# Optimization experiments

Hardware: AMD Instinct MI355X
Metric: run time of the kernel (lower is better)

The kernel has to match this reference:

```python
import jax, jax.numpy as jnp
import numpy as np

B, K, V, NB = 256, 62, 14522, 28

def setup_inputs() -> dict:
    key = jax.random.key(0)
    ks = jax.random.split(key, 10)
    thetas = jax.random.normal(ks[0], (B, K * 3), dtype=jnp.float32) * 0.2
    bone_lengths_core = jax.random.normal(ks[1], (B, NB), dtype=jnp.float32)
    center_bone_length = jax.random.uniform(ks[2], (B, 1), dtype=jnp.float32) + 0.5
    trans = jax.random.normal(ks[3], (B, 3), dtype=jnp.float32)
    scale = jax.random.uniform(ks[4], (B,), dtype=jnp.float32) + 0.5
    v_template = jax.random.normal(ks[5], (V, 3), dtype=jnp.float32) * 0.05
    t_pose_joints = jax.random.normal(ks[6], (K, 3), dtype=jnp.float32) * 0.1
    weights = jax.nn.softmax(jax.random.normal(ks[7], (V, K), dtype=jnp.float32) * 2.0, axis=1)
    # kinematic tree: parent[i] < i (binary-ish tree), parent[0] unused
    parents = jnp.maximum((jnp.arange(K) - 1) // 2, 0).astype(jnp.int64)
    bone_length_mapper = jax.random.randint(ks[8], (K,), -1, NB).astype(jnp.int64)
    return {"thetas": thetas, "bone_lengths_core": bone_lengths_core,
            "center_bone_length": center_bone_length, "trans": trans, "scale": scale,
            "v_template": v_template, "t_pose_joints": t_pose_joints, "weights": weights,
            "parents": parents, "bone_length_mapper": bone_length_mapper}

def euler2mat(r):
    # r: [N,3] ZYX euler angles -> [N,3,3]
    z, y, x = r[:, 0], r[:, 1], r[:, 2]
    cx, sx = jnp.cos(x), jnp.sin(x)
    cy, sy = jnp.cos(y), jnp.sin(y)
    cz, sz = jnp.cos(z), jnp.sin(z)
    one = jnp.ones_like(x)
    zero = jnp.zeros_like(x)
    Rx = jnp.stack([one, zero, zero, zero, cx, -sx, zero, sx, cx], -1).reshape(-1, 3, 3)
    Ry = jnp.stack([cy, zero, sy, zero, one, zero, -sy, zero, cy], -1).reshape(-1, 3, 3)
    Rz = jnp.stack([cz, -sz, zero, sz, cz, zero, zero, zero, one], -1).reshape(-1, 3, 3)
    return jnp.einsum('nij,njk,nkl->nil', Rz, Ry, Rx)

def _forward(thetas, bone_lengths_core, center_bone_length, trans, scale,
             v_template, t_pose_joints, weights, parents, bone_length_mapper):
    b = thetas.shape[0]
    k = t_pose_joints.shape[0]
    blc = jax.nn.sigmoid(bone_lengths_core / 5.0) * 2.0          # [B,28]
    R = euler2mat(thetas.reshape(-1, 3)).reshape(b, k, 3, 3)      # [B,K,3,3]
    Jt = t_pose_joints                                            # [K,3]
    # per-joint bone-length scale factor [B,K]
    gathered = blc[:, jnp.clip(bone_length_mapper, 0)]            # [B,K]
    factor = jnp.where(bone_length_mapper[None, :] < 0, 1.0, gathered)
    factor = factor.at[:, 1].set(center_bone_length[:, 0])
    factor = factor.at[:, 0].set(1.0)
    # local translations: root uses J0, others scaled offsets to parent
    off = (Jt - Jt[parents])[None] * factor[:, :, None]           # [B,K,3]
    off = off.at[:, 0].set(Jt[0][None])
    # local affines A [B,K,4,4]
    A = jnp.zeros((b, k, 4, 4), dtype=thetas.dtype)
    A = A.at[:, :, :3, :3].set(R)
    A = A.at[:, :, :3, 3].set(off)
    A = A.at[:, :, 3, 3].set(1.0)
    # compose along the kinematic tree
    G0 = jnp.zeros_like(A).at[:, 0].set(A[:, 0])
    def step(G_all, i):
        Gp = jnp.take(G_all, parents[i], axis=1)                  # [B,4,4]
        Gi = Gp @ jnp.take(A, i, axis=1)
        return jax.lax.dynamic_update_index_in_dim(G_all, Gi, i, axis=1), None
    G_all, _ = jax.lax.scan(step, G0, jnp.arange(1, k))
    J_final = G_all[:, :, :3, 3]                                  # [B,K,3]
    # subtract inverse-bind contribution: G' = G - pack(G @ [J;0])
    RJ = jnp.einsum('bkij,kj->bki', G_all[:, :, :3, :3], Jt)
    G = G_all.at[:, :, :3, 3].add(-RJ)
    # LBS skinning: T [B,V,4,4]
    T = jnp.einsum('bkij,vk->bvij', G, weights)
    rest_h = jnp.concatenate([v_template, jnp.ones((v_template.shape[0], 1), v_template.dtype)], axis=1)
    v = jnp.einsum('bvij,vj->bvi', T, rest_h)[:, :, :3]
    V_final = v * scale[:, None, None] + trans[:, None, :]
    J_out = J_final * scale[:, None, None] + trans[:, None, :]
    return V_final, J_out

def reference(thetas, bone_lengths_core, center_bone_length, trans, scale,
              v_template, t_pose_joints, weights, parents, bone_length_mapper):
    return _forward(thetas, bone_lengths_core, center_bone_length, trans, scale,
                    v_template, t_pose_joints, weights, parents, bone_length_mapper)
```

## Files before the change

### kernel.cpp

```cpp
#include <hip/hip_runtime.h>

#define NJ     62
#define NV     14522
#define NCORE  28
#define KPAD   256
#define OUTF   (NV * 3)
#define MT     908
#define NSTR   192

typedef __attribute__((ext_vector_type(8))) short short8v;
typedef __attribute__((ext_vector_type(4))) short short4v;
typedef __attribute__((ext_vector_type(4))) float floatx4;
typedef __attribute__((ext_vector_type(2))) float floatx2;

#define AS1(p) ((const __attribute__((address_space(1))) void*)(p))
#define AS3(p) ((__attribute__((address_space(3))) void*)(p))

#define SCHED0() __builtin_amdgcn_sched_barrier(0)
#define WAITVM0() do { SCHED0(); asm volatile("s_waitcnt vmcnt(0)" ::: "memory"); SCHED0(); } while (0)

static __device__ inline short f2bf(float x) {
    unsigned u = __float_as_uint(x);
    unsigned r = (u + 0x7fffu + ((u >> 16) & 1u)) >> 16;
    return (short)r;
}

static __device__ inline short8v pack8(float a0, float a1, float a2, float a3,
                                       float a4, float a5, float a6, float a7) {
    union { unsigned u[4]; short8v v; } p;
    asm("v_cvt_pk_bf16_f32 %0, %1, %2" : "=v"(p.u[0]) : "v"(a0), "v"(a1));
    asm("v_cvt_pk_bf16_f32 %0, %1, %2" : "=v"(p.u[1]) : "v"(a2), "v"(a3));
    asm("v_cvt_pk_bf16_f32 %0, %1, %2" : "=v"(p.u[2]) : "v"(a4), "v"(a5));
    asm("v_cvt_pk_bf16_f32 %0, %1, %2" : "=v"(p.u[3]) : "v"(a6), "v"(a7));
    return p.v;
}

static __device__ inline unsigned swz(unsigned off) {
    return off ^ (((off >> 9) & 7u) << 4);
}

__global__ __launch_bounds__(256) void fk_kernel(
    const float* __restrict__ thetas, const float* __restrict__ blc,
    const float* __restrict__ cbl, const float* __restrict__ trans,
    const float* __restrict__ scale, const float* __restrict__ tpose,
    const int* __restrict__ parents, const int* __restrict__ mapper,
    short* __restrict__ Bt, float* __restrict__ Jout)
{
    __shared__ float Asm[4][NJ][12];
    __shared__ float Gsm[4][NJ][12];

    const int w = threadIdx.x >> 6;
    const int b = blockIdx.x * 4 + w;
    const int k = threadIdx.x & 63;
    int p = 0;

    if (k < NJ) {
        p = parents[k];
        const float tz = thetas[(b * NJ + k) * 3 + 0];
        const float ty = thetas[(b * NJ + k) * 3 + 1];
        const float tx = thetas[(b * NJ + k) * 3 + 2];
        const float cx = cosf(tx), sx = sinf(tx);
        const float cy = cosf(ty), sy = sinf(ty);
        const float cz = cosf(tz), sz = sinf(tz);
        const float r00 = cz * cy;
        const float r01 = cz * sy * sx - sz * cx;
        const float r02 = sz * sx + cz * sy * cx;
        const float r10 = sz * cy;
        const float r11 = cz * cx + sz * sy * sx;
        const float r12 = sz * sy * cx - cz * sx;
        const float r20 = -sy;
        const float r21 = cy * sx;
        const float r22 = cy * cx;

        float f;
        const int m = mapper[k];
        if (k == 0)        f = 1.0f;
        else if (k == 1)   f = cbl[b];
        else if (m < 0)    f = 1.0f;
        else               f = 2.0f / (1.0f + expf(-blc[b * NCORE + m] * 0.2f));

        float ox, oy, oz;
        if (k == 0) {
            ox = tpose[0]; oy = tpose[1]; oz = tpose[2];
        } else {
            ox = (tpose[k * 3 + 0] - tpose[p * 3 + 0]) * f;
            oy = (tpose[k * 3 + 1] - tpose[p * 3 + 1]) * f;
            oz = (tpose[k * 3 + 2] - tpose[p * 3 + 2]) * f;
        }
        Asm[w][k][0] = r00; Asm[w][k][1] = r01; Asm[w][k][2]  = r02; Asm[w][k][3]  = ox;
        Asm[w][k][4] = r10; Asm[w][k][5] = r11; Asm[w][k][6]  = r12; Asm[w][k][7]  = oy;
        Asm[w][k][8] = r20; Asm[w][k][9] = r21; Asm[w][k][10] = r22; Asm[w][k][11] = oz;
    }
    __syncthreads();

    if (k == 0) {
        #pragma unroll
        for (int j = 0; j < 12; ++j) Gsm[w][0][j] = Asm[w][0][j];
    }
    __syncthreads();

    const int depth = (k < NJ) ? (31 - __clz((unsigned)(k + 1))) : 99;
    for (int d = 1; d <= 5; ++d) {
        if (depth == d) {
            float gp[12], a[12], g[12];
            #pragma unroll
            for (int j = 0; j < 12; ++j) { gp[j] = Gsm[w][p][j]; a[j] = Asm[w][k][j]; }
            #pragma unroll
            for (int i = 0; i < 3; ++i) {
                #pragma unroll
                for (int j = 0; j < 4; ++j) {
                    float s = (j == 3) ? gp[i * 4 + 3] : 0.0f;
                    s = fmaf(gp[i * 4 + 0], a[0 * 4 + j], s);
                    s = fmaf(gp[i * 4 + 1], a[1 * 4 + j], s);
                    s = fmaf(gp[i * 4 + 2], a[2 * 4 + j], s);
                    g[i * 4 + j] = s;
                }
            }
            #pragma unroll
            for (int j = 0; j < 12; ++j) Gsm[w][k][j] = g[j];
        }
        __syncthreads();
    }

    if (k < NJ) {
        float g[12];
        #pragma unroll
        for (int j = 0; j < 12; ++j) g[j] = Gsm[w][k][j];
        const float jx = tpose[k * 3 + 0];
        const float jy = tpose[k * 3 + 1];
        const float jz = tpose[k * 3 + 2];
        const float s  = scale[b];
        Jout[(b * NJ + k) * 3 + 0] = fmaf(g[3],  s, trans[b * 3 + 0]);
        Jout[(b * NJ + k) * 3 + 1] = fmaf(g[7],  s, trans[b * 3 + 1]);
        Jout[(b * NJ + k) * 3 + 2] = fmaf(g[11], s, trans[b * 3 + 2]);
        float np[3];
        np[0] = g[3]  - (g[0] * jx + g[1] * jy + g[2]  * jz);
        np[1] = g[7]  - (g[4] * jx + g[5] * jy + g[6]  * jz);
        np[2] = g[11] - (g[8] * jx + g[9] * jy + g[10] * jz);
        #pragma unroll
        for (int i = 0; i < 3; ++i) {
            short4v o;
            o[0] = f2bf(g[i * 4 + 0]);
            o[1] = f2bf(g[i * 4 + 1]);
            o[2] = f2bf(g[i * 4 + 2]);
            o[3] = f2bf(np[i]);
            *(short4v*)&Bt[(size_t)(b * 3 + i) * KPAD + k * 4] = o;
        }
        if (k == 0) {
            short4v z = {0, 0, 0, 0};
            #pragma unroll
            for (int i = 0; i < 3; ++i) {
                *(short4v*)&Bt[(size_t)(b * 3 + i) * KPAD + 248] = z;
                *(short4v*)&Bt[(size_t)(b * 3 + i) * KPAD + 252] = z;
            }
        }
    }
}

__global__ __launch_bounds__(256, 3) void gemm_skin(
    const float* __restrict__ W,
    const float* __restrict__ vt,
    const short* __restrict__ Bt,
    const float* __restrict__ scale,
    const float* __restrict__ trans,
    float* __restrict__ out)
{
    __shared__ __align__(16) char ldsB[48 * 512];
    __shared__ __align__(16) float epi_all[4 * 800];

    const int tid  = threadIdx.x;
    const int wave = tid >> 6;
    const int lane = tid & 63;
    const int lrow = lane & 15;
    const int lk   = lane >> 4;
    const int yy    = blockIdx.x / 48;
    const int inner = blockIdx.x - yy * 48;
    const int s     = inner * 4 + wave;
    const int start  = s * 4 + (s < 140 ? s : 140);
    const int ntiles = 4 + (s < 140 ? 1 : 0);
    const int b0 = yy * 16;
    float* epi = epi_all + wave * 800;

    {
        const char* Bsrc = (const char*)(Bt + (size_t)yy * 48 * KPAD);
        #pragma unroll
        for (int cc = 0; cc < 6; ++cc) {
            const unsigned Lb = (unsigned)(wave * 6144 + cc * 1024);
            __builtin_amdgcn_global_load_lds(AS1(Bsrc + swz(Lb + lane * 16)),
                                             AS3(ldsB + Lb), 16, 0, 0);
        }
    }

    float sv[3], tv[3]; int bl3[3], ii3[3];
    #pragma unroll
    for (int nt = 0; nt < 3; ++nt) {
        const int n_loc = nt * 16 + lrow;
        bl3[nt] = n_loc / 3; ii3[nt] = n_loc - bl3[nt] * 3;
        sv[nt] = scale[b0 + bl3[nt]];
        tv[nt] = trans[(b0 + bl3[nt]) * 3 + ii3[nt]];
    }
    unsigned bofs[3], bxor[3];
    #pragma unroll
    for (int nt = 0; nt < 3; ++nt) {
        const unsigned brow = nt * 16 + lrow;
        bofs[nt] = brow * 512;
        bxor[nt] = (brow & 7u) << 4;
    }

    WAITVM0();
    __syncthreads();

    for (int t = 0; t < ntiles; ++t) {
        const int mtile = start + t;
        int vrow = mtile * 16 + lrow;
        if (vrow > NV - 1) vrow = NV - 1;
        const float hx = vt[vrow * 3 + 0];
        const float hy = vt[vrow * 3 + 1];
        const float hz = vt[vrow * 3 + 2];
        const float* Wr = W + (size_t)vrow * NJ;

        short8v af[8];
        #pragma unroll
        for (int k8 = 0; k8 < 8; ++k8) {
            const int j0 = k8 * 8 + lk * 2;
            float w0 = 0.f, w1 = 0.f;
            if (j0 < NJ) {
                const floatx2 wv = *(const floatx2*)(Wr + j0);
                w0 = wv[0]; w1 = wv[1];
            }
            af[k8] = pack8(w0 * hx, w0 * hy, w0 * hz, w0,
                           w1 * hx, w1 * hy, w1 * hz, w1);
        }

        floatx4 acc[3];
        #pragma unroll
        for (int nt = 0; nt < 3; ++nt) acc[nt] = (floatx4){0.f, 0.f, 0.f, 0.f};
        #pragma unroll
        for (int k8 = 0; k8 < 8; ++k8) {
            const unsigned cb = (unsigned)(k8 * 4 + lk) * 16;
            #pragma unroll
            for (int nt = 0; nt < 3; ++nt) {
                const short8v bf = *(const short8v*)(ldsB + bofs[nt] + (cb ^ bxor[nt]));
                acc[nt] = __builtin_amdgcn_mfma_f32_16x16x32_bf16(
                    af[k8], bf, acc[nt], 0, 0, 0);
            }
        }

        #pragma unroll
        for (int nt = 0; nt < 3; ++nt) {
            #pragma unroll
            for (int r = 0; r < 4; ++r)
                epi[bl3[nt] * 50 + (lk * 4 + r) * 3 + ii3[nt]] =
                    fmaf(acc[nt][r], sv[nt], tv[nt]);
        }

        const int m48 = mtile * 48;
        const bool edge = (m48 + 48 > OUTF);
        #pragma unroll
        for (int it = 0; it < 6; ++it) {
            const int idx = it * 64 + lane;
            const int r = idx / 24, j = idx - r * 24;
            const floatx2 val = *(const floatx2*)&epi[r * 50 + 2 * j];
            const int pp = m48 + 2 * j;
            if (!edge || pp + 1 < OUTF)
                *(floatx2*)&out[(size_t)(b0 + r) * OUTF + pp] = val;
        }
    }
}

extern "C" void kernel_launch(void* const* d_in, const int* in_sizes, int n_in,
                              void* d_out, int out_size, void* d_ws, size_t ws_size,
                              hipStream_t stream)
{
    const float* thetas  = (const float*)d_in[0];
    const float* blc     = (const float*)d_in[1];
    const float* cbl     = (const float*)d_in[2];
    const float* trans   = (const float*)d_in[3];
    const float* scale   = (const float*)d_in[4];
    const float* vtempl  = (const float*)d_in[5];
    const float* tpose   = (const float*)d_in[6];
    const float* weights = (const float*)d_in[7];
    const int*   parents = (const int*)d_in[8];
    const int*   mapper  = (const int*)d_in[9];

    float* out  = (float*)d_out;
    float* Jout = out + (size_t)256 * NV * 3;

    short* Bt = (short*)d_ws;

    fk_kernel<<<64, 256, 0, stream>>>(thetas, blc, cbl, trans, scale, tpose,
                                      parents, mapper, Bt, Jout);
    gemm_skin<<<768, 256, 0, stream>>>(weights, vtempl, Bt, scale, trans, out);
}
```

Before: 26.39 us.

## Permute bone-matrix K layout for vector weight loads and prefetch next tile

```diff
diff --git a/kernel.cpp b/kernel.cpp
--- a/kernel.cpp
+++ b/kernel.cpp
@@ -137,6 +137,10 @@
         np[0] = g[3]  - (g[0] * jx + g[1] * jy + g[2]  * jz);
         np[1] = g[7]  - (g[4] * jx + g[5] * jy + g[6]  * jz);
         np[2] = g[11] - (g[8] * jx + g[9] * jy + g[10] * jz);
+
+        const int lkj = k >> 4;
+        const int rr  = k & 15;
+        const int qb  = 32 * (rr >> 1) + 8 * lkj + 4 * (rr & 1);
         #pragma unroll
         for (int i = 0; i < 3; ++i) {
             short4v o;
@@ -144,7 +148,7 @@
             o[1] = f2bf(g[i * 4 + 1]);
             o[2] = f2bf(g[i * 4 + 2]);
             o[3] = f2bf(np[i]);
-            *(short4v*)&Bt[(size_t)(b * 3 + i) * KPAD + k * 4] = o;
+            *(short4v*)&Bt[(size_t)(b * 3 + i) * KPAD + qb] = o;
         }
         if (k == 0) {
             short4v z = {0, 0, 0, 0};
@@ -191,13 +195,14 @@
         }
     }
 
-    float sv[3], tv[3]; int bl3[3], ii3[3];
+    float sv[3], tv[3]; int eoff[3];
     #pragma unroll
     for (int nt = 0; nt < 3; ++nt) {
         const int n_loc = nt * 16 + lrow;
-        bl3[nt] = n_loc / 3; ii3[nt] = n_loc - bl3[nt] * 3;
-        sv[nt] = scale[b0 + bl3[nt]];
-        tv[nt] = trans[(b0 + bl3[nt]) * 3 + ii3[nt]];
+        const int bl = n_loc / 3, ii = n_loc - bl * 3;
+        eoff[nt] = bl * 50 + ii;
+        sv[nt] = scale[b0 + bl];
+        tv[nt] = trans[(b0 + bl) * 3 + ii];
     }
     unsigned bofs[3], bxor[3];
     #pragma unroll
@@ -207,42 +212,52 @@
         bxor[nt] = (brow & 7u) << 4;
     }
 
+    floatx4 wc[4]; float hcx, hcy, hcz;
+    {
+        int vrow = start * 16 + lrow;
+        if (vrow > NV - 1) vrow = NV - 1;
+        const float* Wb = W + (size_t)vrow * NJ + lk * 16;
+        wc[0] = *(const floatx4*)(Wb + 0);
+        wc[1] = *(const floatx4*)(Wb + 4);
+        wc[2] = *(const floatx4*)(Wb + 8);
+        wc[3] = *(const floatx4*)(Wb + 12);
+        hcx = vt[vrow * 3 + 0]; hcy = vt[vrow * 3 + 1]; hcz = vt[vrow * 3 + 2];
+    }
+
     WAITVM0();
     __syncthreads();
 
     for (int t = 0; t < ntiles; ++t) {
-        const int mtile = start + t;
-        int vrow = mtile * 16 + lrow;
-        if (vrow > NV - 1) vrow = NV - 1;
-        const float hx = vt[vrow * 3 + 0];
-        const float hy = vt[vrow * 3 + 1];
-        const float hz = vt[vrow * 3 + 2];
-        const float* Wr = W + (size_t)vrow * NJ;
-
-        short8v af[8];
+        floatx4 wn[4]; float hnx = 0.f, hny = 0.f, hnz = 0.f;
+        if (t + 1 < ntiles) {
+            int vr = (start + t + 1) * 16 + lrow;
+            if (vr > NV - 1) vr = NV - 1;
+            const float* Wb = W + (size_t)vr * NJ + lk * 16;
+            wn[0] = *(const floatx4*)(Wb + 0);
+            wn[1] = *(const floatx4*)(Wb + 4);
+            wn[2] = *(const floatx4*)(Wb + 8);
+            wn[3] = *(const floatx4*)(Wb + 12);
+            hnx = vt[vr * 3 + 0]; hny = vt[vr * 3 + 1]; hnz = vt[vr * 3 + 2];
+        } else {
+            wn[0] = wn[1] = wn[2] = wn[3] = (floatx4){0.f, 0.f, 0.f, 0.f};
+        }
+
+        floatx4 acc[3];
+        #pragma unroll
+        for (int nt = 0; nt < 3; ++nt) acc[nt] = (floatx4){0.f, 0.f, 0.f, 0.f};
         #pragma unroll
         for (int k8 = 0; k8 < 8; ++k8) {
-            const int j0 = k8 * 8 + lk * 2;
-            float w0 = 0.f, w1 = 0.f;
-            if (j0 < NJ) {
-                const floatx2 wv = *(const floatx2*)(Wr + j0);
-                w0 = wv[0]; w1 = wv[1];
-            }
-            af[k8] = pack8(w0 * hx, w0 * hy, w0 * hz, w0,
-                           w1 * hx, w1 * hy, w1 * hz, w1);
-        }
-
-        floatx4 acc[3];
-        #pragma unroll
-        for (int nt = 0; nt < 3; ++nt) acc[nt] = (floatx4){0.f, 0.f, 0.f, 0.f};
-        #pragma unroll
-        for (int k8 = 0; k8 < 8; ++k8) {
+            float w0 = wc[k8 >> 1][2 * (k8 & 1)];
+            float w1 = wc[k8 >> 1][2 * (k8 & 1) + 1];
+            if (lk == 3 && k8 == 7) { w0 = 0.f; w1 = 0.f; }
+            const short8v a = pack8(w0 * hcx, w0 * hcy, w0 * hcz, w0,
+                                    w1 * hcx, w1 * hcy, w1 * hcz, w1);
             const unsigned cb = (unsigned)(k8 * 4 + lk) * 16;
             #pragma unroll
             for (int nt = 0; nt < 3; ++nt) {
                 const short8v bf = *(const short8v*)(ldsB + bofs[nt] + (cb ^ bxor[nt]));
                 acc[nt] = __builtin_amdgcn_mfma_f32_16x16x32_bf16(
-                    af[k8], bf, acc[nt], 0, 0, 0);
+                    a, bf, acc[nt], 0, 0, 0);
             }
         }
 
@@ -250,11 +265,11 @@
         for (int nt = 0; nt < 3; ++nt) {
             #pragma unroll
             for (int r = 0; r < 4; ++r)
-                epi[bl3[nt] * 50 + (lk * 4 + r) * 3 + ii3[nt]] =
+                epi[eoff[nt] + (lk * 4 + r) * 3] =
                     fmaf(acc[nt][r], sv[nt], tv[nt]);
         }
 
-        const int m48 = mtile * 48;
+        const int m48 = (start + t) * 48;
         const bool edge = (m48 + 48 > OUTF);
         #pragma unroll
         for (int it = 0; it < 6; ++it) {
@@ -265,6 +280,9 @@
             if (!edge || pp + 1 < OUTF)
                 *(floatx2*)&out[(size_t)(b0 + r) * OUTF + pp] = val;
         }
+
+        wc[0] = wn[0]; wc[1] = wn[1]; wc[2] = wn[2]; wc[3] = wn[3];
+        hcx = hnx; hcy = hny; hcz = hnz;
     }
 }
 
```

Result: faster. 25.14 us (-4.7%).
